# Kernel tuning notes

Hardware: AMD Instinct MI355X
Metric: run time of the kernel (lower is better)

## Reference

```python
import jax, jax.numpy as jnp
import numpy as np

EMBED_DIM = 1024
NUM_HEADS = 16
HEAD_DIM = EMBED_DIM // NUM_HEADS
WINDOW = 64


def apply_rope(x):
    # x: (B, H, S, d), rotate-half RoPE with base 10000
    B, H, S, d = x.shape
    half = d // 2
    pos = jnp.arange(S, dtype=x.dtype)
    freqs = 1.0 / (10000.0 ** (jnp.arange(half, dtype=x.dtype) / half))
    ang = pos[:, None] * freqs[None, :]              # (S, half)
    cos, sin = jnp.cos(ang), jnp.sin(ang)
    x1, x2 = x[..., :half], x[..., half:]
    return jnp.concatenate([x1 * cos - x2 * sin, x1 * sin + x2 * cos], axis=-1)


def setup_inputs() -> dict:
    key = jax.random.key(0)
    ks = jax.random.split(key, 12)
    B, S, D = 1, 2048, EMBED_DIM
    scale = 1.0 / np.sqrt(D)
    inp = {
        'query': jax.random.normal(ks[0], (B, S, D), jnp.float32),
        'key':   jax.random.normal(ks[1], (B, S, D), jnp.float32),
        'value': jax.random.normal(ks[2], (B, S, D), jnp.float32),
        'q_w': jax.random.normal(ks[3], (D, D), jnp.float32) * scale,
        'q_b': jax.random.normal(ks[4], (D,), jnp.float32) * 0.01,
        'k_w': jax.random.normal(ks[5], (D, D), jnp.float32) * scale,
        'k_b': jax.random.normal(ks[6], (D,), jnp.float32) * 0.01,
        'v_w': jax.random.normal(ks[7], (D, D), jnp.float32) * scale,
        'v_b': jax.random.normal(ks[8], (D,), jnp.float32) * 0.01,
        'o_w': jax.random.normal(ks[9], (D, D), jnp.float32) * scale,
        'o_b': jax.random.normal(ks[10], (D,), jnp.float32) * 0.01,
    }
    return inp


def _forward(query, key, value, q_w, q_b, k_w, k_b, v_w, v_b, o_w, o_b):
    B, S_q, D = query.shape
    S_k = key.shape[1]
    H, d, W = NUM_HEADS, HEAD_DIM, WINDOW

    q = (query @ q_w.T + q_b).reshape(B, S_q, H, d).transpose(0, 2, 1, 3)
    k = (key   @ k_w.T + k_b).reshape(B, S_k, H, d).transpose(0, 2, 1, 3)
    v = (value @ v_w.T + v_b).reshape(B, S_k, H, d).transpose(0, 2, 1, 3)

    q = apply_rope(q) * (d ** -0.5)
    k = apply_rope(k)

    # window indices: for query i, kv positions i-W .. i (invalid -> masked)
    q_pos = jnp.arange(S_q)[:, None]
    offsets = jnp.arange(-W, 1)[None, :]
    idx = q_pos + offsets                       # (S_q, W+1)
    local_mask = (idx < 0) | (idx >= S_k)       # (S_q, W+1)
    gidx = jnp.clip(idx, 0, S_k - 1)

    k_win = k[:, :, gidx, :]                    # (B, H, S_q, W+1, d)
    v_win = v[:, :, gidx, :]

    scores = jnp.einsum('bhqd,bhqwd->bhqw', q, k_win)
    mask = local_mask[None, None, :, :]
    scores = jnp.where(mask, -jnp.inf, scores)

    # safe softmax: fully-masked rows produce zeros
    m = jnp.max(scores, axis=-1, keepdims=True)
    m = jnp.where(jnp.isfinite(m), m, 0.0)
    e = jnp.exp(scores - m)
    denom = jnp.sum(e, axis=-1, keepdims=True)
    probs = jnp.where(denom > 0, e / jnp.where(denom > 0, denom, 1.0), 0.0)

    ctx = jnp.einsum('bhqw,bhqwd->bhqd', probs, v_win)
    ctx = ctx.transpose(0, 2, 1, 3).reshape(B, S_q, D)
    return ctx @ o_w.T + o_b


def reference(query, key, value, q_w, q_b, k_w, k_b, v_w, v_b, o_w, o_b):
    return _forward(query, key, value, q_w, q_b, k_w, k_b, v_w, v_b, o_w, o_b)
```

## Files before the change

kernel.cpp:

```cpp
#include <hip/hip_runtime.h>
#include <hip/hip_bf16.h>
#include <cstdint>
#include <cstddef>

typedef __attribute__((ext_vector_type(8))) short short8;
typedef __attribute__((ext_vector_type(4))) float f32x4;

__device__ __forceinline__ unsigned short f2bf(float f) {
  union { float f; uint32_t u; } c; c.f = f;
  uint32_t u = c.u;
  u += 0x7fffu + ((u >> 16) & 1u);
  return (unsigned short)(u >> 16);
}

__device__ __forceinline__ void gload16(const void* g, void* l) {
  __builtin_amdgcn_global_load_lds(
      (const __attribute__((address_space(1))) uint32_t*)g,
      (__attribute__((address_space(3))) uint32_t*)l, 16, 0, 0);
}

__global__ __launch_bounds__(256) void cvt_all(
    const float* __restrict__ q, const float* __restrict__ k, const float* __restrict__ v,
    const float* __restrict__ qw, const float* __restrict__ kw,
    const float* __restrict__ vw, const float* __restrict__ ow,
    unsigned short* __restrict__ qb, unsigned short* __restrict__ kb,
    unsigned short* __restrict__ vb, unsigned short* __restrict__ wqb,
    unsigned short* __restrict__ wkb, unsigned short* __restrict__ wvb,
    unsigned short* __restrict__ wob) {
  int i = blockIdx.x * 256 + threadIdx.x;
  const float* src; unsigned short* dst; int off;
  if (i < 1572864) {
    int seg = i >> 19; off = i & 524287;
    src = seg == 0 ? q : seg == 1 ? k : v;
    dst = seg == 0 ? qb : seg == 1 ? kb : vb;
  } else {
    int t = i - 1572864;
    int seg = t >> 18; off = t & 262143;
    src = seg == 0 ? qw : seg == 1 ? kw : seg == 2 ? vw : ow;
    dst = seg == 0 ? wqb : seg == 1 ? wkb : seg == 2 ? wvb : wob;
  }
  float4 x = reinterpret_cast<const float4*>(src)[off];
  ushort4 o;
  o.x = f2bf(x.x); o.y = f2bf(x.y); o.z = f2bf(x.z); o.w = f2bf(x.w);
  reinterpret_cast<ushort4*>(dst)[off] = o;
}

__global__ __launch_bounds__(256) void qkv_gemm(
    const unsigned short* __restrict__ Aq, const unsigned short* __restrict__ Ak,
    const unsigned short* __restrict__ Av,
    const unsigned short* __restrict__ Wq, const unsigned short* __restrict__ Wk,
    const unsigned short* __restrict__ Wv,
    const float* __restrict__ bq, const float* __restrict__ bk,
    const float* __restrict__ bv,
    unsigned short* __restrict__ Oq, unsigned short* __restrict__ Ok,
    unsigned short* __restrict__ OvT) {
  __shared__ __align__(16) unsigned short As[128][32];
  __shared__ __align__(16) unsigned short Bs[128][32];
  const int tid = threadIdx.x;
  const int w = tid >> 6, l = tid & 63;
  const int which = blockIdx.x >> 3;
  const int n0 = (blockIdx.x & 7) * 128;
  const int m0 = blockIdx.y * 128;
  const unsigned short* A = which == 0 ? Aq : which == 1 ? Ak : Av;
  const unsigned short* W = which == 0 ? Wq : which == 1 ? Wk : Wv;

  f32x4 acc[4][4];
#pragma unroll
  for (int a = 0; a < 4; ++a)
#pragma unroll
    for (int b = 0; b < 4; ++b) acc[a][b] = (f32x4){0.f, 0.f, 0.f, 0.f};

  const int wm = w >> 1, wn = w & 1;
  const int lr = l & 15, kq = l >> 4;
  const int srow = tid >> 2;
  const int scol = (tid & 3) * 8;

  for (int kt = 0; kt < 32; ++kt) {
    const int k0 = kt * 32;
    __syncthreads();
    gload16(A + (size_t)(m0 + srow) * 1024 + k0 + scol, (char*)As + tid * 16);
    gload16(A + (size_t)(m0 + 64 + srow) * 1024 + k0 + scol, (char*)As + 4096 + tid * 16);
    gload16(W + (size_t)(n0 + srow) * 1024 + k0 + scol, (char*)Bs + tid * 16);
    gload16(W + (size_t)(n0 + 64 + srow) * 1024 + k0 + scol, (char*)Bs + 4096 + tid * 16);
    __syncthreads();
    short8 af[4], bf[4];
#pragma unroll
    for (int f = 0; f < 4; ++f) {
      af[f] = *reinterpret_cast<const short8*>(&As[wm * 64 + f * 16 + lr][kq * 8]);
      bf[f] = *reinterpret_cast<const short8*>(&Bs[wn * 64 + f * 16 + lr][kq * 8]);
    }
#pragma unroll
    for (int fm = 0; fm < 4; ++fm)
#pragma unroll
      for (int fn = 0; fn < 4; ++fn)
        acc[fm][fn] = __builtin_amdgcn_mfma_f32_16x16x32_bf16(af[fm], bf[fn], acc[fm][fn], 0, 0, 0);
  }

  const float* bias = which == 0 ? bq : which == 1 ? bk : bv;
  if (which < 2) {
    unsigned short* Out = which == 0 ? Oq : Ok;
    const float sc = which == 0 ? 0.125f : 1.0f;
#pragma unroll
    for (int fn = 0; fn < 2; ++fn) {
      const int c1 = n0 + wn * 64 + fn * 16 + lr;
      const int c2 = c1 + 32;
      const int t = fn * 16 + lr;
      const float freq = exp2f(-(float)t * 0.415241012f);
      const float b1 = bias[c1], b2 = bias[c2];
#pragma unroll
      for (int fm = 0; fm < 4; ++fm) {
        const int rbase = m0 + wm * 64 + fm * 16 + kq * 4;
#pragma unroll
        for (int j = 0; j < 4; ++j) {
          const int s = rbase + j;
          float sn, cs;
          __sincosf((float)s * freq, &sn, &cs);
          const float x1 = acc[fm][fn][j] + b1;
          const float x2 = acc[fm][fn + 2][j] + b2;
          Out[(size_t)s * 1024 + c1] = f2bf((x1 * cs - x2 * sn) * sc);
          Out[(size_t)s * 1024 + c2] = f2bf((x1 * sn + x2 * cs) * sc);
        }
      }
    }
  } else {
#pragma unroll
    for (int fn = 0; fn < 4; ++fn) {
      const int c = n0 + wn * 64 + fn * 16 + lr;
      const float bb = bias[c];
#pragma unroll
      for (int fm = 0; fm < 4; ++fm) {
        const int rbase = m0 + wm * 64 + fm * 16 + kq * 4;
        ushort4 o;
        o.x = f2bf(acc[fm][fn][0] + bb);
        o.y = f2bf(acc[fm][fn][1] + bb);
        o.z = f2bf(acc[fm][fn][2] + bb);
        o.w = f2bf(acc[fm][fn][3] + bb);
        *reinterpret_cast<ushort4*>(OvT + (size_t)c * 2048 + rbase) = o;
      }
    }
  }
}

__global__ __launch_bounds__(256) void attn_kernel(
    const unsigned short* __restrict__ qr, const unsigned short* __restrict__ kr,
    const unsigned short* __restrict__ vT, unsigned short* __restrict__ ctx) {
  __shared__ __align__(16) unsigned short Ps[4][16][128];
  const int w = threadIdx.x >> 6, l = threadIdx.x & 63;
  const int h = blockIdx.x & 15, qb = blockIdx.x >> 4;
  const int i0 = qb * 64, hb = h * 64;
  const int r = l & 15, g = l >> 4;

  short8 qf[2];
#pragma unroll
  for (int kk = 0; kk < 2; ++kk)
    qf[kk] = *reinterpret_cast<const short8*>(
        qr + (size_t)(i0 + w * 16 + r) * 1024 + hb + kk * 32 + g * 8);

  f32x4 acc[8];
#pragma unroll
  for (int nt = 0; nt < 8; ++nt) acc[nt] = (f32x4){0.f, 0.f, 0.f, 0.f};
#pragma unroll
  for (int nt = 0; nt < 8; ++nt) {
    int kpos = i0 - 64 + nt * 16 + r;
    int krow = kpos < 0 ? 0 : kpos;
    const unsigned short* kp = kr + (size_t)krow * 1024 + hb + g * 8;
    short8 kf0 = *reinterpret_cast<const short8*>(kp);
    short8 kf1 = *reinterpret_cast<const short8*>(kp + 32);
    acc[nt] = __builtin_amdgcn_mfma_f32_16x16x32_bf16(qf[0], kf0, acc[nt], 0, 0, 0);
    acc[nt] = __builtin_amdgcn_mfma_f32_16x16x32_bf16(qf[1], kf1, acc[nt], 0, 0, 0);
  }

#pragma unroll
  for (int j = 0; j < 4; ++j) {
    const int iq = w * 16 + g * 4 + j;
    float sv[8];
    float m = -1e30f;
#pragma unroll
    for (int nt = 0; nt < 8; ++nt) {
      const int rel = nt * 16 + r - iq;
      const int kpos = i0 - 64 + nt * 16 + r;
      const bool ok = (rel >= 0) && (rel <= 64) && (kpos >= 0);
      sv[nt] = ok ? acc[nt][j] : -1e30f;
      m = fmaxf(m, sv[nt]);
    }
#pragma unroll
    for (int off = 8; off; off >>= 1) m = fmaxf(m, __shfl_xor(m, off));
    float e[8], den = 0.f;
#pragma unroll
    for (int nt = 0; nt < 8; ++nt) { e[nt] = __expf(sv[nt] - m); den += e[nt]; }
#pragma unroll
    for (int off = 8; off; off >>= 1) den += __shfl_xor(den, off);
    const float inv = 1.f / den;
    const int qrow = g * 4 + j;
    const int sw = (qrow & 7) << 3;
#pragma unroll
    for (int nt = 0; nt < 8; ++nt)
      Ps[w][qrow][(nt * 16 + r) ^ sw] = f2bf(e[nt] * inv);
  }

  __syncthreads();

  short8 pf[4];
  const int swr = (r & 7) << 3;
#pragma unroll
  for (int kk = 0; kk < 4; ++kk)
    pf[kk] = *reinterpret_cast<const short8*>(&Ps[w][r][(kk * 32 + g * 8) ^ swr]);

  f32x4 co[4];
#pragma unroll
  for (int n = 0; n < 4; ++n) co[n] = (f32x4){0.f, 0.f, 0.f, 0.f};
#pragma unroll
  for (int kk = 0; kk < 4; ++kk) {
    int cb = i0 - 64 + kk * 32 + g * 8;
    if (cb < 0) cb = 0;
#pragma unroll
    for (int n = 0; n < 4; ++n) {
      short8 vf = *reinterpret_cast<const short8*>(
          vT + (size_t)(hb + n * 16 + r) * 2048 + cb);
      co[n] = __builtin_amdgcn_mfma_f32_16x16x32_bf16(pf[kk], vf, co[n], 0, 0, 0);
    }
  }

#pragma unroll
  for (int n = 0; n < 4; ++n)
#pragma unroll
    for (int j = 0; j < 4; ++j)
      ctx[(size_t)(i0 + w * 16 + g * 4 + j) * 1024 + hb + n * 16 + r] = f2bf(co[n][j]);
}

__global__ __launch_bounds__(256) void oproj_gemm(
    const unsigned short* __restrict__ A, const unsigned short* __restrict__ W,
    const float* __restrict__ bias, float* __restrict__ Out) {
  __shared__ __align__(16) unsigned short As[128][32];
  __shared__ __align__(16) unsigned short Bs[64][32];
  const int tid = threadIdx.x;
  const int w = tid >> 6, l = tid & 63;
  const int n0 = blockIdx.x * 64;
  const int m0 = blockIdx.y * 128;

  f32x4 acc[2][4];
#pragma unroll
  for (int a = 0; a < 2; ++a)
#pragma unroll
    for (int b = 0; b < 4; ++b) acc[a][b] = (f32x4){0.f, 0.f, 0.f, 0.f};

  const int lr = l & 15, kq = l >> 4;
  const int srow = tid >> 2;
  const int scol = (tid & 3) * 8;

  for (int kt = 0; kt < 32; ++kt) {
    const int k0 = kt * 32;
    __syncthreads();
    gload16(A + (size_t)(m0 + srow) * 1024 + k0 + scol, (char*)As + tid * 16);
    gload16(A + (size_t)(m0 + 64 + srow) * 1024 + k0 + scol, (char*)As + 4096 + tid * 16);
    gload16(W + (size_t)(n0 + srow) * 1024 + k0 + scol, (char*)Bs + tid * 16);
    __syncthreads();
    short8 af[2], bf[4];
#pragma unroll
    for (int f = 0; f < 2; ++f)
      af[f] = *reinterpret_cast<const short8*>(&As[w * 32 + f * 16 + lr][kq * 8]);
#pragma unroll
    for (int f = 0; f < 4; ++f)
      bf[f] = *reinterpret_cast<const short8*>(&Bs[f * 16 + lr][kq * 8]);
#pragma unroll
    for (int fm = 0; fm < 2; ++fm)
#pragma unroll
      for (int fn = 0; fn < 4; ++fn)
        acc[fm][fn] = __builtin_amdgcn_mfma_f32_16x16x32_bf16(af[fm], bf[fn], acc[fm][fn], 0, 0, 0);
  }

#pragma unroll
  for (int fm = 0; fm < 2; ++fm) {
    const int rbase = m0 + w * 32 + fm * 16 + kq * 4;
#pragma unroll
    for (int fn = 0; fn < 4; ++fn) {
      const int c = n0 + fn * 16 + lr;
      const float bb = bias[c];
#pragma unroll
      for (int j = 0; j < 4; ++j)
        Out[(size_t)(rbase + j) * 1024 + c] = acc[fm][fn][j] + bb;
    }
  }
}

extern "C" void kernel_launch(void* const* d_in, const int* in_sizes, int n_in,
                              void* d_out, int out_size, void* d_ws, size_t ws_size,
                              hipStream_t stream) {
  const float* query = (const float*)d_in[0];
  const float* key   = (const float*)d_in[1];
  const float* value = (const float*)d_in[2];
  const float* q_w = (const float*)d_in[3];
  const float* q_b = (const float*)d_in[4];
  const float* k_w = (const float*)d_in[5];
  const float* k_b = (const float*)d_in[6];
  const float* v_w = (const float*)d_in[7];
  const float* v_b = (const float*)d_in[8];
  const float* o_w = (const float*)d_in[9];
  const float* o_b = (const float*)d_in[10];
  float* out = (float*)d_out;

  unsigned short* ws = (unsigned short*)d_ws;
  unsigned short* qbf = ws;
  unsigned short* kbf = qbf + 2097152;
  unsigned short* vbf = kbf + 2097152;
  unsigned short* wqb = vbf + 2097152;
  unsigned short* wkb = wqb + 1048576;
  unsigned short* wvb = wkb + 1048576;
  unsigned short* wob = wvb + 1048576;
  unsigned short* qrope = wob + 1048576;
  unsigned short* krope = qrope + 2097152;
  unsigned short* vTb   = krope + 2097152;
  unsigned short* ctxb  = vTb + 2097152;

  cvt_all<<<10240, 256, 0, stream>>>(query, key, value, q_w, k_w, v_w, o_w,
                                     qbf, kbf, vbf, wqb, wkb, wvb, wob);
  qkv_gemm<<<dim3(24, 16), 256, 0, stream>>>(qbf, kbf, vbf, wqb, wkb, wvb,
                                             q_b, k_b, v_b, qrope, krope, vTb);
  attn_kernel<<<512, 256, 0, stream>>>(qrope, krope, vTb, ctxb);
  oproj_gemm<<<dim3(16, 16), 256, 0, stream>>>(ctxb, wob, o_b, out);
}
```

Before: 74.29 us.

## Double-buffer LDS tiles in QKV and output projection GEMMs

Both GEMM kernels now keep two LDS buffers for the A and B tiles. Each iteration issues the global-to-LDS loads for the next k-tile before running the MFMAs on the current tile, and one barrier sits at the end of the iteration instead of two. This is meant to hide global load latency behind matrix-core work. In exchange it doubles LDS use per block, which may lower occupancy, and the end-of-iteration barrier still waits for the prefetch to finish.

```diff
diff --git a/kernel.cpp b/kernel.cpp
--- a/kernel.cpp
+++ b/kernel.cpp
@@ -54,8 +54,8 @@
     const float* __restrict__ bv,
     unsigned short* __restrict__ Oq, unsigned short* __restrict__ Ok,
     unsigned short* __restrict__ OvT) {
-  __shared__ __align__(16) unsigned short As[128][32];
-  __shared__ __align__(16) unsigned short Bs[128][32];
+  __shared__ __align__(16) unsigned short As[2][128][32];
+  __shared__ __align__(16) unsigned short Bs[2][128][32];
   const int tid = threadIdx.x;
   const int w = tid >> 6, l = tid & 63;
   const int which = blockIdx.x >> 3;
@@ -75,25 +75,33 @@
   const int srow = tid >> 2;
   const int scol = (tid & 3) * 8;
 
+  auto stage = [&](int b, int kt) {
+    const int k0 = kt * 32;
+    gload16(A + (size_t)(m0 + srow) * 1024 + k0 + scol, (char*)&As[b][0][0] + tid * 16);
+    gload16(A + (size_t)(m0 + 64 + srow) * 1024 + k0 + scol, (char*)&As[b][0][0] + 4096 + tid * 16);
+    gload16(W + (size_t)(n0 + srow) * 1024 + k0 + scol, (char*)&Bs[b][0][0] + tid * 16);
+    gload16(W + (size_t)(n0 + 64 + srow) * 1024 + k0 + scol, (char*)&Bs[b][0][0] + 4096 + tid * 16);
+  };
+
+  stage(0, 0);
+  __syncthreads();
+
+#pragma unroll 2
   for (int kt = 0; kt < 32; ++kt) {
-    const int k0 = kt * 32;
-    __syncthreads();
-    gload16(A + (size_t)(m0 + srow) * 1024 + k0 + scol, (char*)As + tid * 16);
-    gload16(A + (size_t)(m0 + 64 + srow) * 1024 + k0 + scol, (char*)As + 4096 + tid * 16);
-    gload16(W + (size_t)(n0 + srow) * 1024 + k0 + scol, (char*)Bs + tid * 16);
-    gload16(W + (size_t)(n0 + 64 + srow) * 1024 + k0 + scol, (char*)Bs + 4096 + tid * 16);
-    __syncthreads();
+    const int cur = kt & 1;
+    if (kt < 31) stage(cur ^ 1, kt + 1);
     short8 af[4], bf[4];
 #pragma unroll
     for (int f = 0; f < 4; ++f) {
-      af[f] = *reinterpret_cast<const short8*>(&As[wm * 64 + f * 16 + lr][kq * 8]);
-      bf[f] = *reinterpret_cast<const short8*>(&Bs[wn * 64 + f * 16 + lr][kq * 8]);
+      af[f] = *reinterpret_cast<const short8*>(&As[cur][wm * 64 + f * 16 + lr][kq * 8]);
+      bf[f] = *reinterpret_cast<const short8*>(&Bs[cur][wn * 64 + f * 16 + lr][kq * 8]);
     }
 #pragma unroll
     for (int fm = 0; fm < 4; ++fm)
 #pragma unroll
       for (int fn = 0; fn < 4; ++fn)
         acc[fm][fn] = __builtin_amdgcn_mfma_f32_16x16x32_bf16(af[fm], bf[fn], acc[fm][fn], 0, 0, 0);
+    __syncthreads();
   }
 
   const float* bias = which == 0 ? bq : which == 1 ? bk : bv;
@@ -231,8 +239,8 @@
 __global__ __launch_bounds__(256) void oproj_gemm(
     const unsigned short* __restrict__ A, const unsigned short* __restrict__ W,
     const float* __restrict__ bias, float* __restrict__ Out) {
-  __shared__ __align__(16) unsigned short As[128][32];
-  __shared__ __align__(16) unsigned short Bs[64][32];
+  __shared__ __align__(16) unsigned short As[2][128][32];
+  __shared__ __align__(16) unsigned short Bs[2][64][32];
   const int tid = threadIdx.x;
   const int w = tid >> 6, l = tid & 63;
   const int n0 = blockIdx.x * 64;
@@ -248,25 +256,33 @@
   const int srow = tid >> 2;
   const int scol = (tid & 3) * 8;
 
+  auto stage = [&](int b, int kt) {
+    const int k0 = kt * 32;
+    gload16(A + (size_t)(m0 + srow) * 1024 + k0 + scol, (char*)&As[b][0][0] + tid * 16);
+    gload16(A + (size_t)(m0 + 64 + srow) * 1024 + k0 + scol, (char*)&As[b][0][0] + 4096 + tid * 16);
+    gload16(W + (size_t)(n0 + srow) * 1024 + k0 + scol, (char*)&Bs[b][0][0] + tid * 16);
+  };
+
+  stage(0, 0);
+  __syncthreads();
+
+#pragma unroll 2
   for (int kt = 0; kt < 32; ++kt) {
-    const int k0 = kt * 32;
-    __syncthreads();
-    gload16(A + (size_t)(m0 + srow) * 1024 + k0 + scol, (char*)As + tid * 16);
-    gload16(A + (size_t)(m0 + 64 + srow) * 1024 + k0 + scol, (char*)As + 4096 + tid * 16);
-    gload16(W + (size_t)(n0 + srow) * 1024 + k0 + scol, (char*)Bs + tid * 16);
-    __syncthreads();
+    const int cur = kt & 1;
+    if (kt < 31) stage(cur ^ 1, kt + 1);
     short8 af[2], bf[4];
 #pragma unroll
     for (int f = 0; f < 2; ++f)
-      af[f] = *reinterpret_cast<const short8*>(&As[w * 32 + f * 16 + lr][kq * 8]);
+      af[f] = *reinterpret_cast<const short8*>(&As[cur][w * 32 + f * 16 + lr][kq * 8]);
 #pragma unroll
     for (int f = 0; f < 4; ++f)
-      bf[f] = *reinterpret_cast<const short8*>(&Bs[f * 16 + lr][kq * 8]);
+      bf[f] = *reinterpret_cast<const short8*>(&Bs[cur][f * 16 + lr][kq * 8]);
 #pragma unroll
     for (int fm = 0; fm < 2; ++fm)
 #pragma unroll
       for (int fn = 0; fn < 4; ++fn)
         acc[fm][fn] = __builtin_amdgcn_mfma_f32_16x16x32_bf16(af[fm], bf[fn], acc[fm][fn], 0, 0, 0);
+    __syncthreads();
   }
 
 #pragma unroll
```

Measured after the change: 76.15 us. +2.5%, slower.
